# Kernel tuning notes

Measured on AMD Instinct MI355X. Metric: run time of the kernel, lower is better.

The kernel has to match this reference:

```python
import jax, jax.numpy as jnp
import numpy as np

Q_EPS = 1e-12  # scale clamp used in from_float


def _quantize_rows(w):
    # per-row symmetric int8 quantization: scale = absmax/127, clamp 1e-12
    scales = jnp.clip(jnp.max(jnp.abs(w), axis=1) / 127.0, Q_EPS, None)  # [rows]
    w_i8 = jnp.clip(jnp.round(w / scales[:, None]), -128.0, 127.0)       # int values, fp32 carrier
    return w_i8, scales


def setup_inputs() -> dict:
    key = jax.random.key(0)
    k1, k2, k3 = jax.random.split(key, 3)
    B, S, K, N = 2, 4096, 4096, 4096
    x = jax.random.normal(k1, (B, S, K), dtype=jnp.float32)
    weight_fp = jax.random.normal(k2, (N, K), dtype=jnp.float32) * 0.02
    bias = jax.random.normal(k3, (N,), dtype=jnp.float32) * 0.01
    return {"x": x, "weight_fp": weight_fp, "bias": bias}


def reference(x, weight_fp, bias):
    orig_dtype = x.dtype
    # weight quantization (from_float): per-output-channel scales
    w_i8, w_scales = _quantize_rows(weight_fp)          # [N,K], [N]
    # per-token dynamic activation quantization
    x_shape = x.shape
    x_flat = x.reshape(-1, x_shape[-1])                 # [M,K]
    x_i8, x_scales = _quantize_rows(x_flat)             # [M,K], [M]
    # int8 GEMM accumulated exactly (values fit fp32), fused dequant
    acc = jnp.matmul(x_i8, w_i8.T)                      # [M,N] integer-valued
    out = acc * x_scales[:, None] * w_scales[None, :]
    out = out.astype(jnp.bfloat16)                      # kernel outputs bf16
    out = out.reshape(*x_shape[:-1], w_i8.shape[0])
    out = out + bias.astype(out.dtype)
    return out.astype(orig_dtype)
```

## Files before the change

### kernel.cpp

```cpp
#include <hip/hip_runtime.h>
#include <hip/hip_bf16.h>
#include <stdint.h>


using i32x4 = __attribute__((ext_vector_type(4))) int;

#define TILE 128
#define BK 64

__global__ __launch_bounds__(256) void quant_rows_kernel(
    const float* __restrict__ in, int8_t* __restrict__ qout,
    float* __restrict__ scales, int K)
{
    const int row = blockIdx.x;
    const int tid = threadIdx.x;
    const float* r = in + (size_t)row * K;

    float4 v[4];
#pragma unroll
    for (int j = 0; j < 4; ++j)
        v[j] = *(const float4*)(r + j * 1024 + tid * 4);

    float amax = 0.f;
#pragma unroll
    for (int j = 0; j < 4; ++j) {
        amax = fmaxf(amax, fabsf(v[j].x));
        amax = fmaxf(amax, fabsf(v[j].y));
        amax = fmaxf(amax, fabsf(v[j].z));
        amax = fmaxf(amax, fabsf(v[j].w));
    }

#pragma unroll
    for (int off = 32; off >= 1; off >>= 1)
        amax = fmaxf(amax, __shfl_xor(amax, off));

    __shared__ float red[4];
    const int wave = tid >> 6;
    if ((tid & 63) == 0) red[wave] = amax;
    __syncthreads();
    amax = fmaxf(fmaxf(red[0], red[1]), fmaxf(red[2], red[3]));

    const float scale = fmaxf(amax / 127.0f, 1e-12f);
    if (tid == 0) scales[row] = scale;

#pragma unroll
    for (int j = 0; j < 4; ++j) {
        float q0 = fminf(fmaxf(rintf(v[j].x / scale), -128.f), 127.f);
        float q1 = fminf(fmaxf(rintf(v[j].y / scale), -128.f), 127.f);
        float q2 = fminf(fmaxf(rintf(v[j].z / scale), -128.f), 127.f);
        float q3 = fminf(fmaxf(rintf(v[j].w / scale), -128.f), 127.f);
        union { signed char c[4]; int i; } u;
        u.c[0] = (signed char)(int)q0;
        u.c[1] = (signed char)(int)q1;
        u.c[2] = (signed char)(int)q2;
        u.c[3] = (signed char)(int)q3;
        *(int*)(qout + (size_t)row * K + j * 1024 + tid * 4) = u.i;
    }
}

__global__ __launch_bounds__(256) void gemm_i8_kernel(
    const int8_t* __restrict__ A,
    const int8_t* __restrict__ B,
    const float*  __restrict__ xs,
    const float*  __restrict__ ws,
    const float*  __restrict__ bias,
    float*        __restrict__ out,
    int M, int N, int K)
{
    __shared__ int8_t sA[TILE * BK];
    __shared__ int8_t sB[TILE * BK];

    const int tid  = threadIdx.x;
    const int wave = tid >> 6;
    const int lane = tid & 63;
    const int quad = lane >> 4;
    const int mrow = lane & 15;

    const int bm = blockIdx.y * TILE;
    const int bn = blockIdx.x * TILE;
    const int wm = (wave >> 1) * 64;
    const int wn = (wave & 1) * 64;

    i32x4 acc[4][4];
    const i32x4 zero = {0, 0, 0, 0};
#pragma unroll
    for (int i = 0; i < 4; ++i)
#pragma unroll
        for (int j = 0; j < 4; ++j) acc[i][j] = zero;

    const int srow = tid >> 2;
    const int g    = ((tid & 3) - ((tid >> 3) & 3)) & 3;
    const int soff = g * 16;

    const int8_t* aptr0 = A + (size_t)(bm + srow) * K + soff;
    const int8_t* aptr1 = A + (size_t)(bm + 64 + srow) * K + soff;
    const int8_t* bptr0 = B + (size_t)(bn + srow) * K + soff;
    const int8_t* bptr1 = B + (size_t)(bn + 64 + srow) * K + soff;

    int8_t* sA0 = sA + tid * 16;
    int8_t* sA1 = sA + 4096 + tid * 16;
    int8_t* sB0 = sB + tid * 16;
    int8_t* sB1 = sB + 4096 + tid * 16;

    const int rchunk = ((quad + (mrow >> 1)) & 3) * 16;

    for (int k0 = 0; k0 < K; k0 += BK) {
        __syncthreads();
        __builtin_amdgcn_global_load_lds(
            (const __attribute__((address_space(1))) void*)(aptr0 + k0),
            (__attribute__((address_space(3))) void*)sA0, 16, 0, 0);
        __builtin_amdgcn_global_load_lds(
            (const __attribute__((address_space(1))) void*)(aptr1 + k0),
            (__attribute__((address_space(3))) void*)sA1, 16, 0, 0);
        __builtin_amdgcn_global_load_lds(
            (const __attribute__((address_space(1))) void*)(bptr0 + k0),
            (__attribute__((address_space(3))) void*)sB0, 16, 0, 0);
        __builtin_amdgcn_global_load_lds(
            (const __attribute__((address_space(1))) void*)(bptr1 + k0),
            (__attribute__((address_space(3))) void*)sB1, 16, 0, 0);
        __syncthreads();

        i32x4 af[4], bfr[4];
#pragma unroll
        for (int i = 0; i < 4; ++i)
            af[i] = *(const i32x4*)(sA + (wm + i * 16 + mrow) * BK + rchunk);
#pragma unroll
        for (int j = 0; j < 4; ++j)
            bfr[j] = *(const i32x4*)(sB + (wn + j * 16 + mrow) * BK + rchunk);

#pragma unroll
        for (int i = 0; i < 4; ++i)
#pragma unroll
            for (int j = 0; j < 4; ++j)
                acc[i][j] = __builtin_amdgcn_mfma_i32_16x16x64_i8(
                    af[i], bfr[j], acc[i][j], 0, 0, 0);
    }

#pragma unroll
    for (int j = 0; j < 4; ++j) {
        const int col = bn + wn + j * 16 + mrow;
        const float wsv = ws[col];
        const float bsv = __bfloat162float(__float2bfloat16(bias[col]));
#pragma unroll
        for (int i = 0; i < 4; ++i) {
            const int rowbase = bm + wm + i * 16 + quad * 4;
#pragma unroll
            for (int r = 0; r < 4; ++r) {
                const int row = rowbase + r;
                const float v = (float)acc[i][j][r] * xs[row] * wsv;
                const float vb = __bfloat162float(__float2bfloat16(v));
                const float res = __bfloat162float(__float2bfloat16(vb + bsv));
                out[(size_t)row * N + col] = res;
            }
        }
    }
}

extern "C" void kernel_launch(void* const* d_in, const int* in_sizes, int n_in,
                              void* d_out, int out_size, void* d_ws, size_t ws_size,
                              hipStream_t stream)
{
    const float* x    = (const float*)d_in[0];
    const float* wfp  = (const float*)d_in[1];
    const float* bias = (const float*)d_in[2];
    float* out = (float*)d_out;

    const int N = in_sizes[2];
    const int K = in_sizes[1] / N;
    const int M = in_sizes[0] / K;

    int8_t* w_i8 = (int8_t*)d_ws;
    int8_t* x_i8 = w_i8 + (size_t)N * K;
    float* w_scales = (float*)(x_i8 + (size_t)M * K);
    float* x_scales = w_scales + N;

    quant_rows_kernel<<<N, 256, 0, stream>>>(wfp, w_i8, w_scales, K);
    quant_rows_kernel<<<M, 256, 0, stream>>>(x,   x_i8, x_scales, K);

    dim3 grid(N / TILE, M / TILE);
    gemm_i8_kernel<<<grid, 256, 0, stream>>>(x_i8, w_i8, x_scales, w_scales,
                                             bias, out, M, N, K);
}
```

Measured before the change: 464.5 us.

## Switch int8 GEMM to 32x32x32 MFMA tiles and fuse quantization launches

Replaces the wave's 4x4 grid of 16x16x64 int8 MFMAs with a 2x2 grid of 32x32x32 int8 MFMAs. Each K-step now issues two MFMAs per output tile, with LDS reads re-indexed for the new operand layout and the epilogue row mapping updated. This should cut LDS fragment loads per MFMA and use the larger MFMA shape. Separately, the weight and activation row-quantization kernels merge into one launch to save a launch and let the two tails overlap.

```diff
diff --git a/kernel.cpp b/kernel.cpp
--- a/kernel.cpp
+++ b/kernel.cpp
@@ -3,18 +3,26 @@
 #include <stdint.h>
 
 
-using i32x4 = __attribute__((ext_vector_type(4))) int;
+using i32x4  = __attribute__((ext_vector_type(4))) int;
+using i32x16 = __attribute__((ext_vector_type(16))) int;
 
 #define TILE 128
 #define BK 64
 
-__global__ __launch_bounds__(256) void quant_rows_kernel(
-    const float* __restrict__ in, int8_t* __restrict__ qout,
-    float* __restrict__ scales, int K)
+__global__ __launch_bounds__(256) void quant_rows_fused(
+    const float* __restrict__ w_in, const float* __restrict__ x_in,
+    int8_t* __restrict__ w_q, int8_t* __restrict__ x_q,
+    float* __restrict__ w_s, float* __restrict__ x_s,
+    int nw, int K)
 {
-    const int row = blockIdx.x;
+    const int b   = blockIdx.x;
+    const bool is_w = (b < nw);
+    const int row = is_w ? b : (b - nw);
+    const float* r = (is_w ? w_in : x_in) + (size_t)row * K;
+    int8_t* qout   = (is_w ? w_q : x_q) + (size_t)row * K;
+    float* scales  = is_w ? w_s : x_s;
+
     const int tid = threadIdx.x;
-    const float* r = in + (size_t)row * K;
 
     float4 v[4];
 #pragma unroll
@@ -54,7 +62,7 @@
         u.c[1] = (signed char)(int)q1;
         u.c[2] = (signed char)(int)q2;
         u.c[3] = (signed char)(int)q3;
-        *(int*)(qout + (size_t)row * K + j * 1024 + tid * 4) = u.i;
+        *(int*)(qout + j * 1024 + tid * 4) = u.i;
     }
 }
 
@@ -70,23 +78,24 @@
     __shared__ int8_t sA[TILE * BK];
     __shared__ int8_t sB[TILE * BK];
 
-    const int tid  = threadIdx.x;
-    const int wave = tid >> 6;
-    const int lane = tid & 63;
-    const int quad = lane >> 4;
-    const int mrow = lane & 15;
+    const int tid   = threadIdx.x;
+    const int wave  = tid >> 6;
+    const int lane  = tid & 63;
+    const int l31   = lane & 31;
+    const int lhalf = lane >> 5;
 
     const int bm = blockIdx.y * TILE;
     const int bn = blockIdx.x * TILE;
     const int wm = (wave >> 1) * 64;
     const int wn = (wave & 1) * 64;
 
-    i32x4 acc[4][4];
-    const i32x4 zero = {0, 0, 0, 0};
-#pragma unroll
-    for (int i = 0; i < 4; ++i)
-#pragma unroll
-        for (int j = 0; j < 4; ++j) acc[i][j] = zero;
+    i32x16 acc[2][2];
+#pragma unroll
+    for (int i = 0; i < 2; ++i)
+#pragma unroll
+        for (int j = 0; j < 2; ++j)
+#pragma unroll
+            for (int r = 0; r < 16; ++r) acc[i][j][r] = 0;
 
     const int srow = tid >> 2;
     const int g    = ((tid & 3) - ((tid >> 3) & 3)) & 3;
@@ -102,7 +111,8 @@
     int8_t* sB0 = sB + tid * 16;
     int8_t* sB1 = sB + 4096 + tid * 16;
 
-    const int rchunk = ((quad + (mrow >> 1)) & 3) * 16;
+    const int pc0 = ((lhalf + 0 + (l31 >> 1)) & 3) * 16;
+    const int pc1 = ((lhalf + 2 + (l31 >> 1)) & 3) * 16;
 
     for (int k0 = 0; k0 < K; k0 += BK) {
         __syncthreads();
@@ -120,34 +130,42 @@
             (__attribute__((address_space(3))) void*)sB1, 16, 0, 0);
         __syncthreads();
 
-        i32x4 af[4], bfr[4];
-#pragma unroll
-        for (int i = 0; i < 4; ++i)
-            af[i] = *(const i32x4*)(sA + (wm + i * 16 + mrow) * BK + rchunk);
-#pragma unroll
-        for (int j = 0; j < 4; ++j)
-            bfr[j] = *(const i32x4*)(sB + (wn + j * 16 + mrow) * BK + rchunk);
-
-#pragma unroll
-        for (int i = 0; i < 4; ++i)
-#pragma unroll
-            for (int j = 0; j < 4; ++j)
-                acc[i][j] = __builtin_amdgcn_mfma_i32_16x16x64_i8(
-                    af[i], bfr[j], acc[i][j], 0, 0, 0);
-    }
-
-#pragma unroll
-    for (int j = 0; j < 4; ++j) {
-        const int col = bn + wn + j * 16 + mrow;
+        i32x4 af[2][2], bf[2][2];
+#pragma unroll
+        for (int it = 0; it < 2; ++it) {
+            const int arow = (wm + it * 32 + l31) * BK;
+            af[it][0] = *(const i32x4*)(sA + arow + pc0);
+            af[it][1] = *(const i32x4*)(sA + arow + pc1);
+        }
+#pragma unroll
+        for (int jt = 0; jt < 2; ++jt) {
+            const int brow = (wn + jt * 32 + l31) * BK;
+            bf[jt][0] = *(const i32x4*)(sB + brow + pc0);
+            bf[jt][1] = *(const i32x4*)(sB + brow + pc1);
+        }
+
+#pragma unroll
+        for (int kh = 0; kh < 2; ++kh)
+#pragma unroll
+            for (int it = 0; it < 2; ++it)
+#pragma unroll
+                for (int jt = 0; jt < 2; ++jt)
+                    acc[it][jt] = __builtin_amdgcn_mfma_i32_32x32x32_i8(
+                        af[it][kh], bf[jt][kh], acc[it][jt], 0, 0, 0);
+    }
+
+#pragma unroll
+    for (int jt = 0; jt < 2; ++jt) {
+        const int col = bn + wn + jt * 32 + l31;
         const float wsv = ws[col];
         const float bsv = __bfloat162float(__float2bfloat16(bias[col]));
 #pragma unroll
-        for (int i = 0; i < 4; ++i) {
-            const int rowbase = bm + wm + i * 16 + quad * 4;
-#pragma unroll
-            for (int r = 0; r < 4; ++r) {
-                const int row = rowbase + r;
-                const float v = (float)acc[i][j][r] * xs[row] * wsv;
+        for (int it = 0; it < 2; ++it) {
+            const int rowbase = bm + wm + it * 32 + 4 * lhalf;
+#pragma unroll
+            for (int r = 0; r < 16; ++r) {
+                const int row = rowbase + (r & 3) + 8 * (r >> 2);
+                const float v = (float)acc[it][jt][r] * xs[row] * wsv;
                 const float vb = __bfloat162float(__float2bfloat16(v));
                 const float res = __bfloat162float(__float2bfloat16(vb + bsv));
                 out[(size_t)row * N + col] = res;
@@ -174,8 +192,8 @@
     float* w_scales = (float*)(x_i8 + (size_t)M * K);
     float* x_scales = w_scales + N;
 
-    quant_rows_kernel<<<N, 256, 0, stream>>>(wfp, w_i8, w_scales, K);
-    quant_rows_kernel<<<M, 256, 0, stream>>>(x,   x_i8, x_scales, K);
+    quant_rows_fused<<<N + M, 256, 0, stream>>>(wfp, x, w_i8, x_i8,
+                                                w_scales, x_scales, N, K);
 
     dim3 grid(N / TILE, M / TILE);
     gemm_i8_kernel<<<grid, 256, 0, stream>>>(x_i8, w_i8, x_scales, w_scales,
```

Measured after the change: 441.9 us. -4.9%, faster.
